# Kernel tuning notes

Measured on AMD Instinct MI355X. Metric: run time of the kernel, lower is better.

## Reference

```python
import jax, jax.numpy as jnp
import numpy as np

N_NODES = 50000


def gcn_conv(x, row, col, ew, W, b, n_nodes):
    """PyG GCNConv: add self-loops, symmetric normalization, scatter-add aggregation."""
    loop = jnp.arange(n_nodes)
    r = jnp.concatenate([row, loop])
    c = jnp.concatenate([col, loop])
    w = jnp.concatenate([ew, jnp.ones((n_nodes,), ew.dtype)])
    deg = jax.ops.segment_sum(w, c, num_segments=n_nodes)          # [N]
    dinv = jnp.where(deg > 0, jax.lax.rsqrt(deg), 0.0)
    norm = dinv[r] * w * dinv[c]                                   # [E+N]
    h = x @ W                                                      # [N, out]
    msg = h[r] * norm[:, None]                                     # [E+N, out]
    out = jax.ops.segment_sum(msg, c, num_segments=n_nodes)        # [N, out]
    return out + b


def setup_inputs() -> dict:
    key = jax.random.key(0)
    ks = jax.random.split(key, 7)
    n_feats, hidden, n_classes, n_edges = 256, 128, 40, 800000
    x = jax.random.normal(ks[0], (N_NODES, n_feats), dtype=jnp.float32)
    edge_index = jax.random.randint(ks[1], (2, n_edges), 0, N_NODES, dtype=jnp.int64)
    edge_weight = jax.random.uniform(ks[2], (n_edges,), dtype=jnp.float32)
    # Glorot-ish init for the two GCNConv linear layers (weight stored as [in, out])
    W1 = jax.random.normal(ks[3], (n_feats, hidden), dtype=jnp.float32) * (1.0 / np.sqrt(n_feats))
    b1 = jnp.zeros((hidden,), dtype=jnp.float32)
    W2 = jax.random.normal(ks[4], (hidden, n_classes), dtype=jnp.float32) * (1.0 / np.sqrt(hidden))
    b2 = jnp.zeros((n_classes,), dtype=jnp.float32)
    return {"x": x, "edge_index": edge_index, "edge_weight": edge_weight,
            "W1": W1, "b1": b1, "W2": W2, "b2": b2}


def reference(x, edge_index, edge_weight, W1, b1, W2, b2):
    # Dropout is identity in eval mode.
    row, col = edge_index[0], edge_index[1]
    h = gcn_conv(x, row, col, edge_weight, W1, b1, N_NODES)
    h = jax.nn.relu(h)
    out = gcn_conv(h, row, col, edge_weight, W2, b2, N_NODES)
    return out
```

## Files before the change

### kernel.cpp

```cpp
#include <hip/hip_runtime.h>

#define N_FEATS 256
#define HIDDEN  128
#define NCLASS  40
#define ELLCAP  64

typedef __attribute__((ext_vector_type(8))) short short8;
typedef __attribute__((ext_vector_type(4))) float f32x4;

static __device__ __forceinline__ unsigned short f2bf(float f) {
    unsigned u = __float_as_uint(f);
    u += 0x7fffu + ((u >> 16) & 1u);
    return (unsigned short)(u >> 16);
}
static __device__ __forceinline__ float bflo(unsigned u) { return __uint_as_float(u << 16); }
static __device__ __forceinline__ float bfhi(unsigned u) { return __uint_as_float(u & 0xffff0000u); }

static __device__ __forceinline__ unsigned wq16(float w) {
    float q = w * 65536.0f + 0.5f;
    q = fminf(q, 65535.0f);
    return (unsigned)q;
}
#define WDEQ (1.0f / 65536.0f)

__global__ void k_convW(const float* __restrict__ W1, const float* __restrict__ W2,
                        unsigned short* __restrict__ Wp, unsigned short* __restrict__ Wp2,
                        int* __restrict__ cnt, int N) {
    int idx = blockIdx.x * 256 + threadIdx.x;
    if (idx < N) cnt[idx] = 0;
    if (idx < N_FEATS * HIDDEN) {
        int n = idx >> 8, k = idx & 255;
        Wp[idx] = f2bf(W1[(size_t)k * HIDDEN + n]);
    } else {
        int j = idx - N_FEATS * HIDDEN;
        if (j < 48 * HIDDEN) {
            int n = j >> 7, k = j & 127;
            Wp2[j] = (n < NCLASS) ? f2bf(W2[(size_t)k * NCLASS + n]) : 0;
        }
    }
}

__global__ __launch_bounds__(256) void k_fat(const float* __restrict__ x,
                                             const unsigned short* __restrict__ Wp,
                                             unsigned short* __restrict__ C,
                                             const int* __restrict__ col,
                                             const int* __restrict__ row,
                                             const float* __restrict__ ew,
                                             int* __restrict__ cnt,
                                             unsigned* __restrict__ ed,
                                             int GB, int CB, int N, int E) {
    int bid = blockIdx.x;
    int M = GB < CB ? GB : CB;
    int tile = -1, chunk = -1;
    if (bid < 2 * M) {
        if (bid & 1) chunk = bid >> 1; else tile = bid >> 1;
    } else {
        int r = bid - 2 * M;
        if (GB > CB) tile = M + r; else chunk = M + r;
    }

    if (tile >= 0) {
        __shared__ unsigned short Als[64][72];
        __shared__ unsigned short Bls[128][72];
        int t = threadIdx.x;
        int r0 = tile * 64;
        int wave = t >> 6, lane = t & 63;
        int ml = lane & 15, qd = lane >> 4;

        f32x4 acc[8];
        #pragma unroll
        for (int i = 0; i < 8; ++i) acc[i] = (f32x4){0.f, 0.f, 0.f, 0.f};

        int arow = t >> 2, akg = t & 3;
        int bn = t >> 1, bkg = t & 1;

        for (int k0 = 0; k0 < N_FEATS; k0 += 32) {
            {
                float4 xa0 = make_float4(0.f, 0.f, 0.f, 0.f), xa1 = xa0;
                if (r0 + arow < N) {
                    const float* src = &x[(size_t)(r0 + arow) * N_FEATS + k0 + akg * 8];
                    xa0 = *(const float4*)src;
                    xa1 = *(const float4*)(src + 4);
                }
                short8 av;
                av[0] = (short)f2bf(xa0.x); av[1] = (short)f2bf(xa0.y);
                av[2] = (short)f2bf(xa0.z); av[3] = (short)f2bf(xa0.w);
                av[4] = (short)f2bf(xa1.x); av[5] = (short)f2bf(xa1.y);
                av[6] = (short)f2bf(xa1.z); av[7] = (short)f2bf(xa1.w);
                *(short8*)&Als[arow][akg * 8] = av;
            }
            {
                const short8* src = (const short8*)&Wp[(size_t)bn * N_FEATS + k0 + bkg * 16];
                *(short8*)&Bls[bn][bkg * 16]     = src[0];
                *(short8*)&Bls[bn][bkg * 16 + 8] = src[1];
            }
            __syncthreads();
            short8 af = *(const short8*)&Als[wave * 16 + ml][qd * 8];
            #pragma unroll
            for (int nt = 0; nt < 8; ++nt) {
                short8 bf = *(const short8*)&Bls[nt * 16 + ml][qd * 8];
                acc[nt] = __builtin_amdgcn_mfma_f32_16x16x32_bf16(af, bf, acc[nt], 0, 0, 0);
            }
            __syncthreads();
        }
        #pragma unroll
        for (int nt = 0; nt < 8; ++nt) {
            #pragma unroll
            for (int r = 0; r < 4; ++r) {
                int grow = r0 + wave * 16 + qd * 4 + r;
                if (grow < N)
                    C[(size_t)grow * HIDDEN + nt * 16 + ml] = (unsigned short)f2bf(acc[nt][r]);
            }
        }
    } else {
        int base = chunk * 1024 + threadIdx.x * 4;
        if (base + 4 <= E) {
            int4   c4 = *(const int4*)&col[base];
            int4   r4 = *(const int4*)&row[base];
            float4 w4 = *(const float4*)&ew[base];
            unsigned p0 = ((unsigned)r4.x << 16) | wq16(w4.x);
            unsigned p1 = ((unsigned)r4.y << 16) | wq16(w4.y);
            unsigned p2 = ((unsigned)r4.z << 16) | wq16(w4.z);
            unsigned p3 = ((unsigned)r4.w << 16) | wq16(w4.w);
            int s0 = atomicAdd(&cnt[c4.x], 1);
            int s1 = atomicAdd(&cnt[c4.y], 1);
            int s2 = atomicAdd(&cnt[c4.z], 1);
            int s3 = atomicAdd(&cnt[c4.w], 1);
            if (s0 < ELLCAP) __builtin_nontemporal_store(p0, &ed[((size_t)c4.x << 6) + s0]);
            if (s1 < ELLCAP) __builtin_nontemporal_store(p1, &ed[((size_t)c4.y << 6) + s1]);
            if (s2 < ELLCAP) __builtin_nontemporal_store(p2, &ed[((size_t)c4.z << 6) + s2]);
            if (s3 < ELLCAP) __builtin_nontemporal_store(p3, &ed[((size_t)c4.w << 6) + s3]);
        } else {
            for (int e = base; e < E; ++e) {
                int c = col[e];
                unsigned p = ((unsigned)row[e] << 16) | wq16(ew[e]);
                int s = atomicAdd(&cnt[c], 1);
                if (s < ELLCAP) __builtin_nontemporal_store(p, &ed[((size_t)c << 6) + s]);
            }
        }
    }
}

__global__ void k_degdinv(const int* __restrict__ cnt, const unsigned* __restrict__ ed,
                          float* __restrict__ dinv, int N) {
    int c = blockIdx.x * blockDim.x + threadIdx.x;
    if (c >= N) return;
    int m = cnt[c]; if (m > ELLCAP) m = ELLCAP;
    const unsigned* ep = ed + ((size_t)c << 6);
    unsigned s = 0;
    for (int p = 0; p < m; ++p) s += ep[p] & 0xffffu;
    dinv[c] = rsqrtf(1.0f + (float)s * WDEQ);
}

__global__ __launch_bounds__(256) void k_gather1(const int* __restrict__ cnt,
                                                 const unsigned* __restrict__ ed,
                                                 const unsigned short* __restrict__ h,
                                                 const float* __restrict__ dinv,
                                                 const float* __restrict__ b1,
                                                 const unsigned short* __restrict__ Wp2,
                                                 unsigned short* __restrict__ h2b, int N) {
    __shared__ unsigned short Ah[16][136];
    int t = threadIdx.x;
    int c0 = blockIdx.x * 16;
    int node = t >> 4;
    int c = c0 + node;
    int lane = t & 15;
    const uint4* hb = (const uint4*)h;

    short8 ov = {};
    if (c < N) {
        int m = cnt[c]; if (m > ELLCAP) m = ELLCAP;
        const unsigned* ep = ed + ((size_t)c << 6);
        float acc[8] = {};
        int i = 0;
        for (; i + 8 <= m; i += 8) {
            unsigned e[8];
            uint4 v[8];
            float w[8];
            #pragma unroll
            for (int j = 0; j < 8; ++j) e[j] = ep[i + j];
            #pragma unroll
            for (int j = 0; j < 8; ++j) v[j] = hb[(size_t)(e[j] >> 16) * 16 + lane];
            #pragma unroll
            for (int j = 0; j < 8; ++j) w[j] = (float)(e[j] & 0xffffu) * WDEQ * dinv[e[j] >> 16];
            #pragma unroll
            for (int j = 0; j < 8; ++j) {
                acc[0] += w[j] * bflo(v[j].x); acc[1] += w[j] * bfhi(v[j].x);
                acc[2] += w[j] * bflo(v[j].y); acc[3] += w[j] * bfhi(v[j].y);
                acc[4] += w[j] * bflo(v[j].z); acc[5] += w[j] * bfhi(v[j].z);
                acc[6] += w[j] * bflo(v[j].w); acc[7] += w[j] * bfhi(v[j].w);
            }
        }
        for (; i < m; ++i) {
            unsigned e0 = ep[i];
            uint4 v0 = hb[(size_t)(e0 >> 16) * 16 + lane];
            float w0 = (float)(e0 & 0xffffu) * WDEQ * dinv[e0 >> 16];
            acc[0] += w0 * bflo(v0.x); acc[1] += w0 * bfhi(v0.x);
            acc[2] += w0 * bflo(v0.y); acc[3] += w0 * bfhi(v0.y);
            acc[4] += w0 * bflo(v0.z); acc[5] += w0 * bfhi(v0.z);
            acc[6] += w0 * bflo(v0.w); acc[7] += w0 * bfhi(v0.w);
        }
        float dc = dinv[c], sl = dc * dc;
        uint4 hv = hb[(size_t)c * 16 + lane];
        float4 ba = *(const float4*)&b1[lane * 8];
        float4 bb = *(const float4*)&b1[lane * 8 + 4];
        float o[8];
        o[0] = dc * acc[0] + sl * bflo(hv.x) + ba.x;
        o[1] = dc * acc[1] + sl * bfhi(hv.x) + ba.y;
        o[2] = dc * acc[2] + sl * bflo(hv.y) + ba.z;
        o[3] = dc * acc[3] + sl * bfhi(hv.y) + ba.w;
        o[4] = dc * acc[4] + sl * bflo(hv.z) + bb.x;
        o[5] = dc * acc[5] + sl * bfhi(hv.z) + bb.y;
        o[6] = dc * acc[6] + sl * bflo(hv.w) + bb.z;
        o[7] = dc * acc[7] + sl * bfhi(hv.w) + bb.w;
        #pragma unroll
        for (int j = 0; j < 8; ++j) {
            float v = o[j] > 0.f ? o[j] : 0.f;
            ov[j] = (short)f2bf(v);
        }
    }
    *(short8*)&Ah[node][lane * 8] = ov;
    __syncthreads();

    if (t < 64) {
        int ml = t & 15, qd = t >> 4;
        f32x4 acc2[3];
        #pragma unroll
        for (int i = 0; i < 3; ++i) acc2[i] = (f32x4){0.f, 0.f, 0.f, 0.f};
        #pragma unroll
        for (int ks = 0; ks < 4; ++ks) {
            short8 af = *(const short8*)&Ah[ml][ks * 32 + qd * 8];
            #pragma unroll
            for (int nt = 0; nt < 3; ++nt) {
                short8 bf = *(const short8*)&Wp2[(size_t)(nt * 16 + ml) * HIDDEN + ks * 32 + qd * 8];
                acc2[nt] = __builtin_amdgcn_mfma_f32_16x16x32_bf16(af, bf, acc2[nt], 0, 0, 0);
            }
        }
        #pragma unroll
        for (int nt = 0; nt < 3; ++nt) {
            int j = nt * 16 + ml;
            if (j >= NCLASS) continue;
            #pragma unroll
            for (int r = 0; r < 4; ++r) {
                int gr = c0 + qd * 4 + r;
                if (gr < N) h2b[(size_t)gr * NCLASS + j] = (unsigned short)f2bf(acc2[nt][r]);
            }
        }
    }
}

__global__ __launch_bounds__(256) void k_gather2(const int* __restrict__ cnt,
                                                 const unsigned* __restrict__ ed,
                                                 const unsigned short* __restrict__ h,
                                                 const float* __restrict__ dinv,
                                                 const float* __restrict__ b2,
                                                 float* __restrict__ out, int N) {
    int g = blockIdx.x * blockDim.x + threadIdx.x;
    int c = g / 5;
    if (c >= N) return;
    int part = g - c * 5;
    const uint4* hb = (const uint4*)h;
    int m = cnt[c]; if (m > ELLCAP) m = ELLCAP;
    const unsigned* ep = ed + ((size_t)c << 6);
    float acc[8] = {};
    int i = 0;
    for (; i + 4 <= m; i += 4) {
        unsigned e0 = ep[i], e1 = ep[i + 1], e2 = ep[i + 2], e3 = ep[i + 3];
        uint4 v0 = hb[(size_t)(e0 >> 16) * 5 + part];
        uint4 v1 = hb[(size_t)(e1 >> 16) * 5 + part];
        uint4 v2 = hb[(size_t)(e2 >> 16) * 5 + part];
        uint4 v3 = hb[(size_t)(e3 >> 16) * 5 + part];
        float w0 = (float)(e0 & 0xffffu) * WDEQ * dinv[e0 >> 16];
        float w1 = (float)(e1 & 0xffffu) * WDEQ * dinv[e1 >> 16];
        float w2 = (float)(e2 & 0xffffu) * WDEQ * dinv[e2 >> 16];
        float w3 = (float)(e3 & 0xffffu) * WDEQ * dinv[e3 >> 16];
        acc[0] += w0 * bflo(v0.x); acc[1] += w0 * bfhi(v0.x);
        acc[2] += w0 * bflo(v0.y); acc[3] += w0 * bfhi(v0.y);
        acc[4] += w0 * bflo(v0.z); acc[5] += w0 * bfhi(v0.z);
        acc[6] += w0 * bflo(v0.w); acc[7] += w0 * bfhi(v0.w);
        acc[0] += w1 * bflo(v1.x); acc[1] += w1 * bfhi(v1.x);
        acc[2] += w1 * bflo(v1.y); acc[3] += w1 * bfhi(v1.y);
        acc[4] += w1 * bflo(v1.z); acc[5] += w1 * bfhi(v1.z);
        acc[6] += w1 * bflo(v1.w); acc[7] += w1 * bfhi(v1.w);
        acc[0] += w2 * bflo(v2.x); acc[1] += w2 * bfhi(v2.x);
        acc[2] += w2 * bflo(v2.y); acc[3] += w2 * bfhi(v2.y);
        acc[4] += w2 * bflo(v2.z); acc[5] += w2 * bfhi(v2.z);
        acc[6] += w2 * bflo(v2.w); acc[7] += w2 * bfhi(v2.w);
        acc[0] += w3 * bflo(v3.x); acc[1] += w3 * bfhi(v3.x);
        acc[2] += w3 * bflo(v3.y); acc[3] += w3 * bfhi(v3.y);
        acc[4] += w3 * bflo(v3.z); acc[5] += w3 * bfhi(v3.z);
        acc[6] += w3 * bflo(v3.w); acc[7] += w3 * bfhi(v3.w);
    }
    for (; i < m; ++i) {
        unsigned e0 = ep[i];
        uint4 v0 = hb[(size_t)(e0 >> 16) * 5 + part];
        float w0 = (float)(e0 & 0xffffu) * WDEQ * dinv[e0 >> 16];
        acc[0] += w0 * bflo(v0.x); acc[1] += w0 * bfhi(v0.x);
        acc[2] += w0 * bflo(v0.y); acc[3] += w0 * bfhi(v0.y);
        acc[4] += w0 * bflo(v0.z); acc[5] += w0 * bfhi(v0.z);
        acc[6] += w0 * bflo(v0.w); acc[7] += w0 * bfhi(v0.w);
    }
    float dc = dinv[c], sl = dc * dc;
    uint4 hv = hb[(size_t)c * 5 + part];
    float4 ba = *(const float4*)&b2[part * 8];
    float4 bb = *(const float4*)&b2[part * 8 + 4];
    float4 oa, ob;
    oa.x = dc * acc[0] + sl * bflo(hv.x) + ba.x;
    oa.y = dc * acc[1] + sl * bfhi(hv.x) + ba.y;
    oa.z = dc * acc[2] + sl * bflo(hv.y) + ba.z;
    oa.w = dc * acc[3] + sl * bfhi(hv.y) + ba.w;
    ob.x = dc * acc[4] + sl * bflo(hv.z) + bb.x;
    ob.y = dc * acc[5] + sl * bfhi(hv.z) + bb.y;
    ob.z = dc * acc[6] + sl * bflo(hv.w) + bb.z;
    ob.w = dc * acc[7] + sl * bfhi(hv.w) + bb.w;
    *(float4*)&out[(size_t)c * NCLASS + part * 8]     = oa;
    *(float4*)&out[(size_t)c * NCLASS + part * 8 + 4] = ob;
}

extern "C" void kernel_launch(void* const* d_in, const int* in_sizes, int n_in,
                              void* d_out, int out_size, void* d_ws, size_t ws_size,
                              hipStream_t stream) {
    const float* x  = (const float*)d_in[0];
    const int*   ei = (const int*)d_in[1];
    const float* ew = (const float*)d_in[2];
    const float* W1 = (const float*)d_in[3];
    const float* b1 = (const float*)d_in[4];
    const float* W2 = (const float*)d_in[5];
    const float* b2 = (const float*)d_in[6];
    float* out = (float*)d_out;

    const int E = in_sizes[2];
    const int N = in_sizes[0] / N_FEATS;
    const int* row = ei;
    const int* col = ei + E;

    float* dinv = (float*)d_ws;
    int*   cnt  = (int*)(dinv + N);
    size_t ed_off = ((size_t)(2 * N) + 3) & ~(size_t)3;
    unsigned* ed = (unsigned*)((int*)d_ws + ed_off);
    unsigned short* Wp  = (unsigned short*)(ed + (size_t)N * ELLCAP);
    unsigned short* Wp2 = Wp + (size_t)N_FEATS * HIDDEN;
    unsigned short* h1b = Wp2 + 48 * HIDDEN;
    unsigned short* h2b = h1b + (size_t)N * HIDDEN;

    {
        int nw = N_FEATS * HIDDEN + 48 * HIDDEN;
        int total = N > nw ? N : nw;
        k_convW<<<(total + 255) / 256, 256, 0, stream>>>(W1, W2, Wp, Wp2, cnt, N);
    }

    {
        int GB = (N + 63) / 64;
        int CB = (E + 1023) / 1024;
        k_fat<<<GB + CB, 256, 0, stream>>>(x, Wp, h1b, col, row, ew, cnt, ed, GB, CB, N, E);
    }

    k_degdinv<<<(N + 255) / 256, 256, 0, stream>>>(cnt, ed, dinv, N);

    k_gather1<<<(N + 15) / 16, 256, 0, stream>>>(cnt, ed, h1b, dinv, b1, Wp2, h2b, N);

    k_gather2<<<((N * 5) + 255) / 256, 256, 0, stream>>>(cnt, ed, h2b, dinv, b2, out, N);
}
```

Measured before the change: 199.5 us.

## Pack degree into 64-bit atomic counter and use wave-per-node gathers

Each edge scatter now adds its quantized weight into the high bits of a 64-bit per-node counter, so the degree sum arrives with the slot count. The degree kernel no longer rereads the ELL rows. Both gather kernels switch to one wave per node: lanes split the edge list and combine partial sums with xor shuffles. The hidden-2 buffer is padded to 48 columns so each row is 16-byte aligned for vector loads. This adds 64-bit atomics and cross-lane reductions, and some lanes stay idle in the second gather.

```diff
diff --git a/kernel.cpp b/kernel.cpp
--- a/kernel.cpp
+++ b/kernel.cpp
@@ -3,6 +3,7 @@
 #define N_FEATS 256
 #define HIDDEN  128
 #define NCLASS  40
+#define H2PAD   48
 #define ELLCAP  64
 
 typedef __attribute__((ext_vector_type(8))) short short8;
@@ -25,15 +26,15 @@
 
 __global__ void k_convW(const float* __restrict__ W1, const float* __restrict__ W2,
                         unsigned short* __restrict__ Wp, unsigned short* __restrict__ Wp2,
-                        int* __restrict__ cnt, int N) {
+                        unsigned long long* __restrict__ cntw, int N) {
     int idx = blockIdx.x * 256 + threadIdx.x;
-    if (idx < N) cnt[idx] = 0;
+    if (idx < N) cntw[idx] = 0ull;
     if (idx < N_FEATS * HIDDEN) {
         int n = idx >> 8, k = idx & 255;
         Wp[idx] = f2bf(W1[(size_t)k * HIDDEN + n]);
     } else {
         int j = idx - N_FEATS * HIDDEN;
-        if (j < 48 * HIDDEN) {
+        if (j < H2PAD * HIDDEN) {
             int n = j >> 7, k = j & 127;
             Wp2[j] = (n < NCLASS) ? f2bf(W2[(size_t)k * NCLASS + n]) : 0;
         }
@@ -46,7 +47,7 @@
                                              const int* __restrict__ col,
                                              const int* __restrict__ row,
                                              const float* __restrict__ ew,
-                                             int* __restrict__ cnt,
+                                             unsigned long long* __restrict__ cntw,
                                              unsigned* __restrict__ ed,
                                              int GB, int CB, int N, int E) {
     int bid = blockIdx.x;
@@ -118,14 +119,19 @@
             int4   c4 = *(const int4*)&col[base];
             int4   r4 = *(const int4*)&row[base];
             float4 w4 = *(const float4*)&ew[base];
-            unsigned p0 = ((unsigned)r4.x << 16) | wq16(w4.x);
-            unsigned p1 = ((unsigned)r4.y << 16) | wq16(w4.y);
-            unsigned p2 = ((unsigned)r4.z << 16) | wq16(w4.z);
-            unsigned p3 = ((unsigned)r4.w << 16) | wq16(w4.w);
-            int s0 = atomicAdd(&cnt[c4.x], 1);
-            int s1 = atomicAdd(&cnt[c4.y], 1);
-            int s2 = atomicAdd(&cnt[c4.z], 1);
-            int s3 = atomicAdd(&cnt[c4.w], 1);
+            unsigned q0 = wq16(w4.x), q1 = wq16(w4.y), q2 = wq16(w4.z), q3 = wq16(w4.w);
+            unsigned p0 = ((unsigned)r4.x << 16) | q0;
+            unsigned p1 = ((unsigned)r4.y << 16) | q1;
+            unsigned p2 = ((unsigned)r4.z << 16) | q2;
+            unsigned p3 = ((unsigned)r4.w << 16) | q3;
+            unsigned long long a0 = atomicAdd(&cntw[c4.x], ((unsigned long long)q0 << 20) | 1ull);
+            unsigned long long a1 = atomicAdd(&cntw[c4.y], ((unsigned long long)q1 << 20) | 1ull);
+            unsigned long long a2 = atomicAdd(&cntw[c4.z], ((unsigned long long)q2 << 20) | 1ull);
+            unsigned long long a3 = atomicAdd(&cntw[c4.w], ((unsigned long long)q3 << 20) | 1ull);
+            int s0 = (int)(a0 & 0xFFFFFu);
+            int s1 = (int)(a1 & 0xFFFFFu);
+            int s2 = (int)(a2 & 0xFFFFFu);
+            int s3 = (int)(a3 & 0xFFFFFu);
             if (s0 < ELLCAP) __builtin_nontemporal_store(p0, &ed[((size_t)c4.x << 6) + s0]);
             if (s1 < ELLCAP) __builtin_nontemporal_store(p1, &ed[((size_t)c4.y << 6) + s1]);
             if (s2 < ELLCAP) __builtin_nontemporal_store(p2, &ed[((size_t)c4.z << 6) + s2]);
@@ -133,77 +139,89 @@
         } else {
             for (int e = base; e < E; ++e) {
                 int c = col[e];
-                unsigned p = ((unsigned)row[e] << 16) | wq16(ew[e]);
-                int s = atomicAdd(&cnt[c], 1);
+                unsigned q = wq16(ew[e]);
+                unsigned p = ((unsigned)row[e] << 16) | q;
+                unsigned long long a = atomicAdd(&cntw[c], ((unsigned long long)q << 20) | 1ull);
+                int s = (int)(a & 0xFFFFFu);
                 if (s < ELLCAP) __builtin_nontemporal_store(p, &ed[((size_t)c << 6) + s]);
             }
         }
     }
 }
 
-__global__ void k_degdinv(const int* __restrict__ cnt, const unsigned* __restrict__ ed,
-                          float* __restrict__ dinv, int N) {
+__global__ void k_degdinv(const unsigned long long* __restrict__ cntw,
+                          float* __restrict__ dinv, int* __restrict__ cnt, int N) {
     int c = blockIdx.x * blockDim.x + threadIdx.x;
     if (c >= N) return;
-    int m = cnt[c]; if (m > ELLCAP) m = ELLCAP;
-    const unsigned* ep = ed + ((size_t)c << 6);
-    unsigned s = 0;
-    for (int p = 0; p < m; ++p) s += ep[p] & 0xffffu;
-    dinv[c] = rsqrtf(1.0f + (float)s * WDEQ);
-}
-
-__global__ __launch_bounds__(256) void k_gather1(const int* __restrict__ cnt,
-                                                 const unsigned* __restrict__ ed,
-                                                 const unsigned short* __restrict__ h,
-                                                 const float* __restrict__ dinv,
-                                                 const float* __restrict__ b1,
-                                                 const unsigned short* __restrict__ Wp2,
-                                                 unsigned short* __restrict__ h2b, int N) {
+    unsigned long long v = cntw[c];
+    int m = (int)(v & 0xFFFFFu); if (m > ELLCAP) m = ELLCAP;
+    cnt[c] = m;
+    dinv[c] = rsqrtf(1.0f + (float)(v >> 20) * WDEQ);
+}
+
+__global__ __launch_bounds__(1024) void k_gather1(const int* __restrict__ cnt,
+                                                  const unsigned* __restrict__ ed,
+                                                  const unsigned short* __restrict__ h,
+                                                  const float* __restrict__ dinv,
+                                                  const float* __restrict__ b1,
+                                                  const unsigned short* __restrict__ Wp2,
+                                                  unsigned short* __restrict__ h2b, int N) {
     __shared__ unsigned short Ah[16][136];
     int t = threadIdx.x;
+    int wave = t >> 6, lane = t & 63;
+    int g = lane >> 4, f = lane & 15;
     int c0 = blockIdx.x * 16;
-    int node = t >> 4;
-    int c = c0 + node;
-    int lane = t & 15;
+    int c = c0 + wave;
     const uint4* hb = (const uint4*)h;
 
+    float acc[8] = {};
     short8 ov = {};
     if (c < N) {
-        int m = cnt[c]; if (m > ELLCAP) m = ELLCAP;
+        int m = cnt[c];
         const unsigned* ep = ed + ((size_t)c << 6);
-        float acc[8] = {};
         int i = 0;
         for (; i + 8 <= m; i += 8) {
-            unsigned e[8];
-            uint4 v[8];
-            float w[8];
-            #pragma unroll
-            for (int j = 0; j < 8; ++j) e[j] = ep[i + j];
-            #pragma unroll
-            for (int j = 0; j < 8; ++j) v[j] = hb[(size_t)(e[j] >> 16) * 16 + lane];
-            #pragma unroll
-            for (int j = 0; j < 8; ++j) w[j] = (float)(e[j] & 0xffffu) * WDEQ * dinv[e[j] >> 16];
-            #pragma unroll
-            for (int j = 0; j < 8; ++j) {
-                acc[0] += w[j] * bflo(v[j].x); acc[1] += w[j] * bfhi(v[j].x);
-                acc[2] += w[j] * bflo(v[j].y); acc[3] += w[j] * bfhi(v[j].y);
-                acc[4] += w[j] * bflo(v[j].z); acc[5] += w[j] * bfhi(v[j].z);
-                acc[6] += w[j] * bflo(v[j].w); acc[7] += w[j] * bfhi(v[j].w);
-            }
-        }
-        for (; i < m; ++i) {
-            unsigned e0 = ep[i];
-            uint4 v0 = hb[(size_t)(e0 >> 16) * 16 + lane];
+            unsigned e0 = ep[i + g], e1 = ep[i + g + 4];
+            uint4 v0 = hb[(size_t)(e0 >> 16) * 16 + f];
+            uint4 v1 = hb[(size_t)(e1 >> 16) * 16 + f];
+            float w0 = (float)(e0 & 0xffffu) * WDEQ * dinv[e0 >> 16];
+            float w1 = (float)(e1 & 0xffffu) * WDEQ * dinv[e1 >> 16];
+            acc[0] += w0 * bflo(v0.x); acc[1] += w0 * bfhi(v0.x);
+            acc[2] += w0 * bflo(v0.y); acc[3] += w0 * bfhi(v0.y);
+            acc[4] += w0 * bflo(v0.z); acc[5] += w0 * bfhi(v0.z);
+            acc[6] += w0 * bflo(v0.w); acc[7] += w0 * bfhi(v0.w);
+            acc[0] += w1 * bflo(v1.x); acc[1] += w1 * bfhi(v1.x);
+            acc[2] += w1 * bflo(v1.y); acc[3] += w1 * bfhi(v1.y);
+            acc[4] += w1 * bflo(v1.z); acc[5] += w1 * bfhi(v1.z);
+            acc[6] += w1 * bflo(v1.w); acc[7] += w1 * bfhi(v1.w);
+        }
+        if (i + g < m) {
+            unsigned e0 = ep[i + g];
+            uint4 v0 = hb[(size_t)(e0 >> 16) * 16 + f];
             float w0 = (float)(e0 & 0xffffu) * WDEQ * dinv[e0 >> 16];
             acc[0] += w0 * bflo(v0.x); acc[1] += w0 * bfhi(v0.x);
             acc[2] += w0 * bflo(v0.y); acc[3] += w0 * bfhi(v0.y);
             acc[4] += w0 * bflo(v0.z); acc[5] += w0 * bfhi(v0.z);
             acc[6] += w0 * bflo(v0.w); acc[7] += w0 * bfhi(v0.w);
         }
+        if (i + g + 4 < m) {
+            unsigned e1 = ep[i + g + 4];
+            uint4 v1 = hb[(size_t)(e1 >> 16) * 16 + f];
+            float w1 = (float)(e1 & 0xffffu) * WDEQ * dinv[e1 >> 16];
+            acc[0] += w1 * bflo(v1.x); acc[1] += w1 * bfhi(v1.x);
+            acc[2] += w1 * bflo(v1.y); acc[3] += w1 * bfhi(v1.y);
+            acc[4] += w1 * bflo(v1.z); acc[5] += w1 * bfhi(v1.z);
+            acc[6] += w1 * bflo(v1.w); acc[7] += w1 * bfhi(v1.w);
+        }
+        #pragma unroll
+        for (int j = 0; j < 8; ++j) acc[j] += __shfl_xor(acc[j], 16, 64);
+        #pragma unroll
+        for (int j = 0; j < 8; ++j) acc[j] += __shfl_xor(acc[j], 32, 64);
+
         float dc = dinv[c], sl = dc * dc;
-        uint4 hv = hb[(size_t)c * 16 + lane];
-        float4 ba = *(const float4*)&b1[lane * 8];
-        float4 bb = *(const float4*)&b1[lane * 8 + 4];
+        uint4 hv = hb[(size_t)c * 16 + f];
+        float4 ba = *(const float4*)&b1[f * 8];
+        float4 bb = *(const float4*)&b1[f * 8 + 4];
         float o[8];
         o[0] = dc * acc[0] + sl * bflo(hv.x) + ba.x;
         o[1] = dc * acc[1] + sl * bfhi(hv.x) + ba.y;
@@ -219,7 +237,7 @@
             ov[j] = (short)f2bf(v);
         }
     }
-    *(short8*)&Ah[node][lane * 8] = ov;
+    if (g == 0) *(short8*)&Ah[wave][f * 8] = ov;
     __syncthreads();
 
     if (t < 64) {
@@ -239,11 +257,10 @@
         #pragma unroll
         for (int nt = 0; nt < 3; ++nt) {
             int j = nt * 16 + ml;
-            if (j >= NCLASS) continue;
             #pragma unroll
             for (int r = 0; r < 4; ++r) {
                 int gr = c0 + qd * 4 + r;
-                if (gr < N) h2b[(size_t)gr * NCLASS + j] = (unsigned short)f2bf(acc2[nt][r]);
+                if (gr < N) h2b[(size_t)gr * H2PAD + j] = (unsigned short)f2bf(acc2[nt][r]);
             }
         }
     }
@@ -255,66 +272,80 @@
                                                  const float* __restrict__ dinv,
                                                  const float* __restrict__ b2,
                                                  float* __restrict__ out, int N) {
-    int g = blockIdx.x * blockDim.x + threadIdx.x;
-    int c = g / 5;
+    int t = threadIdx.x;
+    int wave = t >> 6, lane = t & 63;
+    int g = lane >> 3, s = lane & 7;
+    int c = blockIdx.x * 4 + wave;
     if (c >= N) return;
-    int part = g - c * 5;
     const uint4* hb = (const uint4*)h;
-    int m = cnt[c]; if (m > ELLCAP) m = ELLCAP;
+    bool act = s < 6;
+    int m = cnt[c];
     const unsigned* ep = ed + ((size_t)c << 6);
     float acc[8] = {};
     int i = 0;
-    for (; i + 4 <= m; i += 4) {
-        unsigned e0 = ep[i], e1 = ep[i + 1], e2 = ep[i + 2], e3 = ep[i + 3];
-        uint4 v0 = hb[(size_t)(e0 >> 16) * 5 + part];
-        uint4 v1 = hb[(size_t)(e1 >> 16) * 5 + part];
-        uint4 v2 = hb[(size_t)(e2 >> 16) * 5 + part];
-        uint4 v3 = hb[(size_t)(e3 >> 16) * 5 + part];
+    for (; i + 16 <= m; i += 16) {
+        unsigned e0 = ep[i + g], e1 = ep[i + g + 8];
         float w0 = (float)(e0 & 0xffffu) * WDEQ * dinv[e0 >> 16];
         float w1 = (float)(e1 & 0xffffu) * WDEQ * dinv[e1 >> 16];
-        float w2 = (float)(e2 & 0xffffu) * WDEQ * dinv[e2 >> 16];
-        float w3 = (float)(e3 & 0xffffu) * WDEQ * dinv[e3 >> 16];
-        acc[0] += w0 * bflo(v0.x); acc[1] += w0 * bfhi(v0.x);
-        acc[2] += w0 * bflo(v0.y); acc[3] += w0 * bfhi(v0.y);
-        acc[4] += w0 * bflo(v0.z); acc[5] += w0 * bfhi(v0.z);
-        acc[6] += w0 * bflo(v0.w); acc[7] += w0 * bfhi(v0.w);
-        acc[0] += w1 * bflo(v1.x); acc[1] += w1 * bfhi(v1.x);
-        acc[2] += w1 * bflo(v1.y); acc[3] += w1 * bfhi(v1.y);
-        acc[4] += w1 * bflo(v1.z); acc[5] += w1 * bfhi(v1.z);
-        acc[6] += w1 * bflo(v1.w); acc[7] += w1 * bfhi(v1.w);
-        acc[0] += w2 * bflo(v2.x); acc[1] += w2 * bfhi(v2.x);
-        acc[2] += w2 * bflo(v2.y); acc[3] += w2 * bfhi(v2.y);
-        acc[4] += w2 * bflo(v2.z); acc[5] += w2 * bfhi(v2.z);
-        acc[6] += w2 * bflo(v2.w); acc[7] += w2 * bfhi(v2.w);
-        acc[0] += w3 * bflo(v3.x); acc[1] += w3 * bfhi(v3.x);
-        acc[2] += w3 * bflo(v3.y); acc[3] += w3 * bfhi(v3.y);
-        acc[4] += w3 * bflo(v3.z); acc[5] += w3 * bfhi(v3.z);
-        acc[6] += w3 * bflo(v3.w); acc[7] += w3 * bfhi(v3.w);
-    }
-    for (; i < m; ++i) {
-        unsigned e0 = ep[i];
-        uint4 v0 = hb[(size_t)(e0 >> 16) * 5 + part];
+        if (act) {
+            uint4 v0 = hb[(size_t)(e0 >> 16) * 6 + s];
+            uint4 v1 = hb[(size_t)(e1 >> 16) * 6 + s];
+            acc[0] += w0 * bflo(v0.x); acc[1] += w0 * bfhi(v0.x);
+            acc[2] += w0 * bflo(v0.y); acc[3] += w0 * bfhi(v0.y);
+            acc[4] += w0 * bflo(v0.z); acc[5] += w0 * bfhi(v0.z);
+            acc[6] += w0 * bflo(v0.w); acc[7] += w0 * bfhi(v0.w);
+            acc[0] += w1 * bflo(v1.x); acc[1] += w1 * bfhi(v1.x);
+            acc[2] += w1 * bflo(v1.y); acc[3] += w1 * bfhi(v1.y);
+            acc[4] += w1 * bflo(v1.z); acc[5] += w1 * bfhi(v1.z);
+            acc[6] += w1 * bflo(v1.w); acc[7] += w1 * bfhi(v1.w);
+        }
+    }
+    if (i + g < m) {
+        unsigned e0 = ep[i + g];
         float w0 = (float)(e0 & 0xffffu) * WDEQ * dinv[e0 >> 16];
-        acc[0] += w0 * bflo(v0.x); acc[1] += w0 * bfhi(v0.x);
-        acc[2] += w0 * bflo(v0.y); acc[3] += w0 * bfhi(v0.y);
-        acc[4] += w0 * bflo(v0.z); acc[5] += w0 * bfhi(v0.z);
-        acc[6] += w0 * bflo(v0.w); acc[7] += w0 * bfhi(v0.w);
-    }
-    float dc = dinv[c], sl = dc * dc;
-    uint4 hv = hb[(size_t)c * 5 + part];
-    float4 ba = *(const float4*)&b2[part * 8];
-    float4 bb = *(const float4*)&b2[part * 8 + 4];
-    float4 oa, ob;
-    oa.x = dc * acc[0] + sl * bflo(hv.x) + ba.x;
-    oa.y = dc * acc[1] + sl * bfhi(hv.x) + ba.y;
-    oa.z = dc * acc[2] + sl * bflo(hv.y) + ba.z;
-    oa.w = dc * acc[3] + sl * bfhi(hv.y) + ba.w;
-    ob.x = dc * acc[4] + sl * bflo(hv.z) + bb.x;
-    ob.y = dc * acc[5] + sl * bfhi(hv.z) + bb.y;
-    ob.z = dc * acc[6] + sl * bflo(hv.w) + bb.z;
-    ob.w = dc * acc[7] + sl * bfhi(hv.w) + bb.w;
-    *(float4*)&out[(size_t)c * NCLASS + part * 8]     = oa;
-    *(float4*)&out[(size_t)c * NCLASS + part * 8 + 4] = ob;
+        if (act) {
+            uint4 v0 = hb[(size_t)(e0 >> 16) * 6 + s];
+            acc[0] += w0 * bflo(v0.x); acc[1] += w0 * bfhi(v0.x);
+            acc[2] += w0 * bflo(v0.y); acc[3] += w0 * bfhi(v0.y);
+            acc[4] += w0 * bflo(v0.z); acc[5] += w0 * bfhi(v0.z);
+            acc[6] += w0 * bflo(v0.w); acc[7] += w0 * bfhi(v0.w);
+        }
+    }
+    if (i + g + 8 < m) {
+        unsigned e1 = ep[i + g + 8];
+        float w1 = (float)(e1 & 0xffffu) * WDEQ * dinv[e1 >> 16];
+        if (act) {
+            uint4 v1 = hb[(size_t)(e1 >> 16) * 6 + s];
+            acc[0] += w1 * bflo(v1.x); acc[1] += w1 * bfhi(v1.x);
+            acc[2] += w1 * bflo(v1.y); acc[3] += w1 * bfhi(v1.y);
+            acc[4] += w1 * bflo(v1.z); acc[5] += w1 * bfhi(v1.z);
+            acc[6] += w1 * bflo(v1.w); acc[7] += w1 * bfhi(v1.w);
+        }
+    }
+    #pragma unroll
+    for (int j = 0; j < 8; ++j) acc[j] += __shfl_xor(acc[j], 8, 64);
+    #pragma unroll
+    for (int j = 0; j < 8; ++j) acc[j] += __shfl_xor(acc[j], 16, 64);
+    #pragma unroll
+    for (int j = 0; j < 8; ++j) acc[j] += __shfl_xor(acc[j], 32, 64);
+
+    if (g == 0 && s < 5) {
+        float dc = dinv[c], sl = dc * dc;
+        uint4 hv = hb[(size_t)c * 6 + s];
+        float4 ba = *(const float4*)&b2[s * 8];
+        float4 bb = *(const float4*)&b2[s * 8 + 4];
+        float4 oa, ob;
+        oa.x = dc * acc[0] + sl * bflo(hv.x) + ba.x;
+        oa.y = dc * acc[1] + sl * bfhi(hv.x) + ba.y;
+        oa.z = dc * acc[2] + sl * bflo(hv.y) + ba.z;
+        oa.w = dc * acc[3] + sl * bfhi(hv.y) + ba.w;
+        ob.x = dc * acc[4] + sl * bflo(hv.z) + bb.x;
+        ob.y = dc * acc[5] + sl * bfhi(hv.z) + bb.y;
+        ob.z = dc * acc[6] + sl * bflo(hv.w) + bb.z;
+        ob.w = dc * acc[7] + sl * bfhi(hv.w) + bb.w;
+        *(float4*)&out[(size_t)c * NCLASS + s * 8]     = oa;
+        *(float4*)&out[(size_t)c * NCLASS + s * 8 + 4] = ob;
+    }
 }
 
 extern "C" void kernel_launch(void* const* d_in, const int* in_sizes, int n_in,
@@ -334,30 +365,30 @@
     const int* row = ei;
     const int* col = ei + E;
 
-    float* dinv = (float*)d_ws;
+    unsigned long long* cntw = (unsigned long long*)d_ws;
+    float* dinv = (float*)(cntw + N);
     int*   cnt  = (int*)(dinv + N);
-    size_t ed_off = ((size_t)(2 * N) + 3) & ~(size_t)3;
-    unsigned* ed = (unsigned*)((int*)d_ws + ed_off);
+    unsigned* ed = (unsigned*)(cnt + N);
     unsigned short* Wp  = (unsigned short*)(ed + (size_t)N * ELLCAP);
     unsigned short* Wp2 = Wp + (size_t)N_FEATS * HIDDEN;
-    unsigned short* h1b = Wp2 + 48 * HIDDEN;
+    unsigned short* h1b = Wp2 + H2PAD * HIDDEN;
     unsigned short* h2b = h1b + (size_t)N * HIDDEN;
 
     {
-        int nw = N_FEATS * HIDDEN + 48 * HIDDEN;
+        int nw = N_FEATS * HIDDEN + H2PAD * HIDDEN;
         int total = N > nw ? N : nw;
-        k_convW<<<(total + 255) / 256, 256, 0, stream>>>(W1, W2, Wp, Wp2, cnt, N);
+        k_convW<<<(total + 255) / 256, 256, 0, stream>>>(W1, W2, Wp, Wp2, cntw, N);
     }
 
     {
         int GB = (N + 63) / 64;
         int CB = (E + 1023) / 1024;
-        k_fat<<<GB + CB, 256, 0, stream>>>(x, Wp, h1b, col, row, ew, cnt, ed, GB, CB, N, E);
-    }
-
-    k_degdinv<<<(N + 255) / 256, 256, 0, stream>>>(cnt, ed, dinv, N);
-
-    k_gather1<<<(N + 15) / 16, 256, 0, stream>>>(cnt, ed, h1b, dinv, b1, Wp2, h2b, N);
-
-    k_gather2<<<((N * 5) + 255) / 256, 256, 0, stream>>>(cnt, ed, h2b, dinv, b2, out, N);
-}
+        k_fat<<<GB + CB, 256, 0, stream>>>(x, Wp, h1b, col, row, ew, cntw, ed, GB, CB, N, E);
+    }
+
+    k_degdinv<<<(N + 255) / 256, 256, 0, stream>>>(cntw, dinv, cnt, N);
+
+    k_gather1<<<(N + 15) / 16, 1024, 0, stream>>>(cnt, ed, h1b, dinv, b1, Wp2, h2b, N);
+
+    k_gather2<<<(N + 3) / 4, 256, 0, stream>>>(cnt, ed, h2b, dinv, b2, out, N);
+}
```

New measurement: 204.1 us. +2.3%, slower.
